# Optimization experiments

Hardware: AMD Instinct MI355X
Metric: run time of the kernel (lower is better)

Reference implementation:

```python
import jax, jax.numpy as jnp
import numpy as np

B, S, H = 32, 4096, 1024


def setup_inputs() -> dict:
    key = jax.random.key(0)
    ks = jax.random.split(key, 6)
    sc = 1.0 / np.sqrt(H)
    return {
        "hidden_state": jax.random.normal(ks[0], (B, 1, H), dtype=jnp.float32),
        "encoder_outputs": jax.random.normal(ks[1], (B, S, H), dtype=jnp.float32),
        "A_w": jax.random.normal(ks[2], (H, H), dtype=jnp.float32) * sc,
        "A_b": jax.random.normal(ks[3], (H,), dtype=jnp.float32) * 0.01,
        "C_w": jax.random.normal(ks[4], (H, 2 * H), dtype=jnp.float32) * sc,
        "C_b": jax.random.normal(ks[5], (H,), dtype=jnp.float32) * 0.01,
    }


def reference(hidden_state, encoder_outputs, A_w, A_b, C_w, C_b):
    # NOTE: source applies A twice to hidden_state (first reassignment, then
    # again inside the bmm). We reproduce that exactly.
    h1 = hidden_state @ A_w.T + A_b            # [B,1,H] (reassigned hidden_state)
    h2 = h1 @ A_w.T + A_b                      # second A application for scores
    scores = jnp.einsum('bsh,bqh->bsq', encoder_outputs, h2)   # [B,S,1]
    attn = jax.nn.softmax(scores, axis=1)                      # softmax over S
    context = jnp.einsum('bsq,bsh->bqh', attn, encoder_outputs)  # [B,1,H]
    concat = jnp.concatenate([h1[:, 0], context[:, 0]], axis=1)  # [B,2H]
    out = jnp.tanh(concat @ C_w.T + C_b)                         # [B,H]
    return out, attn
```

## Files before the change

kernel.cpp:

```cpp
#include <hip/hip_runtime.h>
#include <math.h>

#define B_ 32
#define S_ 4096
#define H_ 1024

#define RPB   128
#define NBLK  (S_ / RPB)
#define RPW   32
#define NTIL  16

__device__ __forceinline__ float wave_reduce_sum(float v) {
    #pragma unroll
    for (int o = 32; o > 0; o >>= 1) v += __shfl_xor(v, o, 64);
    return v;
}

__global__ __launch_bounds__(256) void gemv_aw(const float* __restrict__ x, int xstride,
                                               const float* __restrict__ W,
                                               const float* __restrict__ bias,
                                               float* __restrict__ y, int ystride) {
    int w = threadIdx.x >> 6, lane = threadIdx.x & 63;
    int gw = blockIdx.x * 4 + w;
    int b = gw >> 10, i = gw & 1023;
    const float4* xr = reinterpret_cast<const float4*>(x + (size_t)b * xstride);
    const float4* wr = reinterpret_cast<const float4*>(W + (size_t)i * H_);
    float s = 0.f;
    #pragma unroll
    for (int k = 0; k < 4; ++k) {
        float4 a = xr[lane + k * 64];
        float4 ww = wr[lane + k * 64];
        s += a.x * ww.x + a.y * ww.y + a.z * ww.z + a.w * ww.w;
    }
    s = wave_reduce_sum(s);
    if (lane == 0) y[(size_t)b * ystride + i] = s + bias[i];
}

#define LOADROW(dst, row) do {                                                   \
    const float4* rp_ = reinterpret_cast<const float4*>(encb + (size_t)(row) * H_); \
    dst[0] = rp_[lane]; dst[1] = rp_[lane + 64];                                 \
    dst[2] = rp_[lane + 128]; dst[3] = rp_[lane + 192];                          \
} while (0)

#define PROCESS(va, vb, lr) do {                                                 \
    float s0 = 0.f, s1 = 0.f;                                                    \
    _Pragma("unroll")                                                            \
    for (int k = 0; k < 4; ++k) {                                                \
        s0 += va[k].x * hv[k].x + va[k].y * hv[k].y + va[k].z * hv[k].z + va[k].w * hv[k].w; \
        s1 += vb[k].x * hv[k].x + vb[k].y * hv[k].y + vb[k].z * hv[k].z + vb[k].w * hv[k].w; \
    }                                                                            \
    s0 = wave_reduce_sum(s0);                                                    \
    s1 = wave_reduce_sum(s1);                                                    \
    my_score = (lane == (lr)    ) ? s0 : my_score;                               \
    my_score = (lane == (lr) + 1) ? s1 : my_score;                               \
    float tm_ = fmaxf(s0, s1);                                                   \
    if (tm_ > m) {                                       \
        float sc_ = __expf(m - tm_);          \
        l *= sc_;                                                                \
        _Pragma("unroll")                                                        \
        for (int k = 0; k < 4; ++k) {                                            \
            acc[k].x *= sc_; acc[k].y *= sc_; acc[k].z *= sc_; acc[k].w *= sc_;  \
        }                                                                        \
        m = tm_;                                                                 \
    }                                                                            \
    float p0_ = __expf(s0 - m), p1_ = __expf(s1 - m);                            \
    l += p0_ + p1_;                                                              \
    _Pragma("unroll")                                                            \
    for (int k = 0; k < 4; ++k) {                                                \
        acc[k].x += p0_ * va[k].x + p1_ * vb[k].x;                               \
        acc[k].y += p0_ * va[k].y + p1_ * vb[k].y;                               \
        acc[k].z += p0_ * va[k].z + p1_ * vb[k].z;                               \
        acc[k].w += p0_ * va[k].w + p1_ * vb[k].w;                               \
    }                                                                            \
} while (0)

__global__ __launch_bounds__(256, 3) void attn_pass1(const float* __restrict__ enc,
                                                     const float* __restrict__ h2,
                                                     float* __restrict__ scores,
                                                     float* __restrict__ partials) {
    int b   = blockIdx.x >> 5;
    int blk = blockIdx.x & (NBLK - 1);
    int w = threadIdx.x >> 6, lane = threadIdx.x & 63;

    const float* encb = enc + (size_t)b * S_ * H_;

    const float4* hp = reinterpret_cast<const float4*>(h2 + (size_t)b * H_);
    float4 hv[4];
    #pragma unroll
    for (int k = 0; k < 4; ++k) hv[k] = hp[lane + k * 64];

    float m = -INFINITY, l = 0.f;
    float4 acc[4];
    #pragma unroll
    for (int k = 0; k < 4; ++k) acc[k] = make_float4(0.f, 0.f, 0.f, 0.f);

    int row0 = blk * RPB + w * RPW;
    float my_score = 0.f;

    float4 A0[4], A1[4], B0[4], B1[4];
    LOADROW(A0, row0);
    LOADROW(A1, row0 + 1);

    #pragma unroll
    for (int t = 0; t < NTIL; t += 2) {
        LOADROW(B0, row0 + 2 * t + 2);
        LOADROW(B1, row0 + 2 * t + 3);
        PROCESS(A0, A1, 2 * t);
        if (t + 2 < NTIL) {
            LOADROW(A0, row0 + 2 * t + 4);
            LOADROW(A1, row0 + 2 * t + 5);
        }
        PROCESS(B0, B1, 2 * t + 2);
    }
    if (lane < RPW) scores[(size_t)b * S_ + row0 + lane] = my_score;

    __shared__ float lds_ctx[4][H_];
    __shared__ float lds_m[4], lds_l[4];
    float4* mc = reinterpret_cast<float4*>(&lds_ctx[w][0]);
    #pragma unroll
    for (int k = 0; k < 4; ++k) mc[lane + k * 64] = acc[k];
    if (lane == 0) { lds_m[w] = m; lds_l[w] = l; }
    __syncthreads();

    float mb = fmaxf(fmaxf(lds_m[0], lds_m[1]), fmaxf(lds_m[2], lds_m[3]));
    float sc0 = __expf(lds_m[0] - mb), sc1 = __expf(lds_m[1] - mb);
    float sc2 = __expf(lds_m[2] - mb), sc3 = __expf(lds_m[3] - mb);
    float lb = lds_l[0] * sc0 + lds_l[1] * sc1 + lds_l[2] * sc2 + lds_l[3] * sc3;

    float* part = partials + ((size_t)b * NBLK + blk) * (H_ + 2);
    #pragma unroll
    for (int k2 = 0; k2 < 4; ++k2) {
        int col = threadIdx.x + k2 * 256;
        float v = lds_ctx[0][col] * sc0 + lds_ctx[1][col] * sc1 +
                  lds_ctx[2][col] * sc2 + lds_ctx[3][col] * sc3;
        part[2 + col] = v;
    }
    if (threadIdx.x == 0) { part[0] = mb; part[1] = lb; }
}

__global__ __launch_bounds__(256) void attn_reduce(const float* __restrict__ partials,
                                                   float* __restrict__ concat,
                                                   const float* __restrict__ scores,
                                                   float* __restrict__ attn_out) {
    int b = blockIdx.x >> 2;
    int q = blockIdx.x & 3;
    const float* part = partials + (size_t)b * NBLK * (H_ + 2);
    float ms[NBLK];
    float mb = -INFINITY;
    #pragma unroll
    for (int k = 0; k < NBLK; ++k) {
        ms[k] = part[(size_t)k * (H_ + 2)];
        mb = fmaxf(mb, ms[k]);
    }
    float lb = 0.f;
    float sc[NBLK];
    #pragma unroll
    for (int k = 0; k < NBLK; ++k) {
        sc[k] = __expf(ms[k] - mb);
        lb += part[(size_t)k * (H_ + 2) + 1] * sc[k];
    }
    float inv_l = 1.f / lb;
    int col = q * 256 + threadIdx.x;
    float v = 0.f;
    #pragma unroll
    for (int k = 0; k < NBLK; ++k)
        v += part[(size_t)k * (H_ + 2) + 2 + col] * sc[k];
    concat[(size_t)b * 2048 + 1024 + col] = v * inv_l;

    const float4* sp = reinterpret_cast<const float4*>(scores + (size_t)b * S_ + q * 1024);
    float4* ap = reinterpret_cast<float4*>(attn_out + (size_t)b * S_ + q * 1024);
    float4 sv = sp[threadIdx.x];
    float4 av;
    av.x = __expf(sv.x - mb) * inv_l;
    av.y = __expf(sv.y - mb) * inv_l;
    av.z = __expf(sv.z - mb) * inv_l;
    av.w = __expf(sv.w - mb) * inv_l;
    ap[threadIdx.x] = av;
}

__global__ __launch_bounds__(256) void out_gemm(const float* __restrict__ concat,
                                                const float* __restrict__ Cw,
                                                const float* __restrict__ Cb,
                                                float* __restrict__ out) {
    int w = threadIdx.x >> 6, lane = threadIdx.x & 63;
    int i = blockIdx.x;
    const float4* wr = reinterpret_cast<const float4*>(Cw + (size_t)i * 2048);
    float4 wv[8];
    #pragma unroll
    for (int k = 0; k < 8; ++k) wv[k] = wr[lane + k * 64];
    float bias = Cb[i];
    #pragma unroll
    for (int bb = 0; bb < 8; ++bb) {
        int b = w * 8 + bb;
        const float4* cr = reinterpret_cast<const float4*>(concat + (size_t)b * 2048);
        float s = 0.f;
        #pragma unroll
        for (int k = 0; k < 8; ++k) {
            float4 c = cr[lane + k * 64];
            s += c.x * wv[k].x + c.y * wv[k].y + c.z * wv[k].z + c.w * wv[k].w;
        }
        s = wave_reduce_sum(s);
        if (lane == 0) out[(size_t)b * H_ + i] = tanhf(s + bias);
    }
}

extern "C" void kernel_launch(void* const* d_in, const int* in_sizes, int n_in,
                              void* d_out, int out_size, void* d_ws, size_t ws_size,
                              hipStream_t stream) {
    const float* hs  = (const float*)d_in[0];
    const float* enc = (const float*)d_in[1];
    const float* A_w = (const float*)d_in[2];
    const float* A_b = (const float*)d_in[3];
    const float* C_w = (const float*)d_in[4];
    const float* C_b = (const float*)d_in[5];

    float* out      = (float*)d_out;
    float* attn_out = out + B_ * H_;

    float* ws       = (float*)d_ws;
    float* concat   = ws;
    float* h2       = ws + (size_t)B_ * 2048;
    float* scores   = h2 + (size_t)B_ * H_;
    float* partials = scores + (size_t)B_ * S_;

    gemv_aw<<<(B_ * H_) / 4, 256, 0, stream>>>(hs, H_, A_w, A_b, concat, 2048);
    gemv_aw<<<(B_ * H_) / 4, 256, 0, stream>>>(concat, 2048, A_w, A_b, h2, H_);
    attn_pass1<<<B_ * NBLK, 256, 0, stream>>>(enc, h2, scores, partials);
    attn_reduce<<<B_ * 4, 256, 0, stream>>>(partials, concat, scores, attn_out);
    out_gemm<<<H_, 256, 0, stream>>>(concat, C_w, C_b, out);
}
```

Measured before the change: 154.5 us.

## Deepen encoder row prefetch to four row pairs in attention pass

```diff
diff --git a/kernel.cpp b/kernel.cpp
--- a/kernel.cpp
+++ b/kernel.cpp
@@ -8,12 +8,19 @@
 #define RPB   128
 #define NBLK  (S_ / RPB)
 #define RPW   32
-#define NTIL  16
 
 __device__ __forceinline__ float wave_reduce_sum(float v) {
     #pragma unroll
     for (int o = 32; o > 0; o >>= 1) v += __shfl_xor(v, o, 64);
     return v;
+}
+
+__device__ __forceinline__ void wave_reduce_sum2(float& a, float& b) {
+    #pragma unroll
+    for (int o = 32; o > 0; o >>= 1) {
+        a += __shfl_xor(a, o, 64);
+        b += __shfl_xor(b, o, 64);
+    }
 }
 
 __global__ __launch_bounds__(256) void gemv_aw(const float* __restrict__ x, int xstride,
@@ -36,10 +43,11 @@
     if (lane == 0) y[(size_t)b * ystride + i] = s + bias[i];
 }
 
-#define LOADROW(dst, row) do {                                                   \
-    const float4* rp_ = reinterpret_cast<const float4*>(encb + (size_t)(row) * H_); \
-    dst[0] = rp_[lane]; dst[1] = rp_[lane + 64];                                 \
-    dst[2] = rp_[lane + 128]; dst[3] = rp_[lane + 192];                          \
+#define LOADPAIR(d0, d1, r) do {                                                 \
+    const float4* rp_ = base + (size_t)(r) * 256;                                \
+    d0[0] = rp_[0]; d0[1] = rp_[64]; d0[2] = rp_[128]; d0[3] = rp_[192];         \
+    const float4* rq_ = rp_ + 256;                                               \
+    d1[0] = rq_[0]; d1[1] = rq_[64]; d1[2] = rq_[128]; d1[3] = rq_[192];         \
 } while (0)
 
 #define PROCESS(va, vb, lr) do {                                                 \
@@ -49,8 +57,7 @@
         s0 += va[k].x * hv[k].x + va[k].y * hv[k].y + va[k].z * hv[k].z + va[k].w * hv[k].w; \
         s1 += vb[k].x * hv[k].x + vb[k].y * hv[k].y + vb[k].z * hv[k].z + vb[k].w * hv[k].w; \
     }                                                                            \
-    s0 = wave_reduce_sum(s0);                                                    \
-    s1 = wave_reduce_sum(s1);                                                    \
+    wave_reduce_sum2(s0, s1);                                                    \
     my_score = (lane == (lr)    ) ? s0 : my_score;                               \
     my_score = (lane == (lr) + 1) ? s1 : my_score;                               \
     float tm_ = fmaxf(s0, s1);                                                   \
@@ -74,7 +81,7 @@
     }                                                                            \
 } while (0)
 
-__global__ __launch_bounds__(256, 3) void attn_pass1(const float* __restrict__ enc,
+__global__ __launch_bounds__(256, 2) void attn_pass1(const float* __restrict__ enc,
                                                      const float* __restrict__ h2,
                                                      float* __restrict__ scores,
                                                      float* __restrict__ partials) {
@@ -82,7 +89,9 @@
     int blk = blockIdx.x & (NBLK - 1);
     int w = threadIdx.x >> 6, lane = threadIdx.x & 63;
 
-    const float* encb = enc + (size_t)b * S_ * H_;
+    int row0 = blk * RPB + w * RPW;
+    const float4* base = reinterpret_cast<const float4*>(
+        enc + (size_t)b * S_ * H_ + (size_t)row0 * H_) + lane;
 
     const float4* hp = reinterpret_cast<const float4*>(h2 + (size_t)b * H_);
     float4 hv[4];
@@ -93,24 +102,24 @@
     float4 acc[4];
     #pragma unroll
     for (int k = 0; k < 4; ++k) acc[k] = make_float4(0.f, 0.f, 0.f, 0.f);
-
-    int row0 = blk * RPB + w * RPW;
     float my_score = 0.f;
 
-    float4 A0[4], A1[4], B0[4], B1[4];
-    LOADROW(A0, row0);
-    LOADROW(A1, row0 + 1);
-
-    #pragma unroll
-    for (int t = 0; t < NTIL; t += 2) {
-        LOADROW(B0, row0 + 2 * t + 2);
-        LOADROW(B1, row0 + 2 * t + 3);
-        PROCESS(A0, A1, 2 * t);
-        if (t + 2 < NTIL) {
-            LOADROW(A0, row0 + 2 * t + 4);
-            LOADROW(A1, row0 + 2 * t + 5);
-        }
-        PROCESS(B0, B1, 2 * t + 2);
+    float4 A0[4], A1[4], B0[4], B1[4], C0[4], C1[4], D0[4], D1[4];
+    LOADPAIR(A0, A1, 0);
+    LOADPAIR(B0, B1, 2);
+    LOADPAIR(C0, C1, 4);
+    LOADPAIR(D0, D1, 6);
+
+    #pragma unroll 1
+    for (int t = 0; t < RPW; t += 8) {
+        PROCESS(A0, A1, t);
+        if (t + 8 < RPW)  LOADPAIR(A0, A1, t + 8);
+        PROCESS(B0, B1, t + 2);
+        if (t + 10 < RPW) LOADPAIR(B0, B1, t + 10);
+        PROCESS(C0, C1, t + 4);
+        if (t + 12 < RPW) LOADPAIR(C0, C1, t + 12);
+        PROCESS(D0, D1, t + 6);
+        if (t + 14 < RPW) LOADPAIR(D0, D1, t + 14);
     }
     if (lane < RPW) scores[(size_t)b * S_ + row0 + lane] = my_score;
 
```

After: 145.2 us. -6.0%, faster.
